# Kernel optimization log

Hardware: AMD Instinct MI355X
Metric: run time of the kernel (lower is better)

## Reference

```python
import jax, jax.numpy as jnp
import numpy as np

N, C, P, K = 100000, 64, 64, 16  # points, in_planes, planes, nsample
EPS = 1e-5

def _bn(y, g, b, m, v):
    # inference-mode batchnorm over channel (last) dim
    return (y - m) * (g * jax.lax.rsqrt(v + EPS)) + b

def setup_inputs() -> dict:
    key = jax.random.key(0)
    ks = jax.random.split(key, 12)
    p = jax.random.normal(ks[0], (N, 3), jnp.float32)
    x = jax.random.normal(ks[1], (N, C), jnp.float32)
    idx = jax.random.randint(ks[2], (N, K), 0, N, jnp.int32)
    s = 0.05
    w1 = jax.random.normal(ks[3], (C, P), jnp.float32) * s
    conv_w = jax.random.normal(ks[4], (P, P + 3), jnp.float32) * s  # Conv1d(P+3, P, 1) weight squeezed
    w3 = jax.random.normal(ks[5], (P, P), jnp.float32) * s
    def bn_params(k):
        k1, k2 = jax.random.split(k)
        return (jnp.ones((P,), jnp.float32),                      # gamma
                jnp.zeros((P,), jnp.float32),                     # beta
                jax.random.normal(k1, (P,), jnp.float32) * 0.01,  # running mean
                jnp.abs(jax.random.normal(k2, (P,), jnp.float32)) * 0.1 + 1.0)  # running var
    g1, b1, m1, v1 = bn_params(ks[6])
    g2, b2, m2, v2 = bn_params(ks[7])
    g3, b3, m3, v3 = bn_params(ks[8])
    return dict(p=p, x=x, idx=idx, w1=w1, g1=g1, b1=b1, m1=m1, v1=v1,
                conv_w=conv_w, g2=g2, b2=b2, m2=m2, v2=v2,
                w3=w3, g3=g3, b3=b3, m3=m3, v3=v3)

def reference(p, x, idx, w1, g1, b1, m1, v1, conv_w, g2, b2, m2, v2, w3, g3, b3, m3, v3):
    identity = x
    h = jax.nn.relu(_bn(x @ w1, g1, b1, m1, v1))                     # [N, P]
    # queryandgroup with use_xyz=True: concat(relative xyz, neighbor feats)
    rel = p[idx] - p[:, None, :]                                      # [N, K, 3]
    grouped = jnp.concatenate([rel, h[idx]], axis=-1)                 # [N, K, 3+P]
    e = jnp.einsum('nkc,oc->nko', grouped, conv_w)                    # conv1x1 -> [N, K, P]
    e = jax.nn.relu(_bn(e, g2, b2, m2, v2))
    f = jnp.max(e, axis=1)                                            # max over neighbors -> [N, P]
    out = jax.nn.relu(_bn(f @ w3, g3, b3, m3, v3) + identity)         # [N, P]
    return out
```

## Files before the change

kernel.cpp:

```cpp
#include <hip/hip_runtime.h>
#include <stdint.h>


#define EPS 1e-5f

typedef unsigned short u16;
typedef unsigned int u32;
typedef __attribute__((ext_vector_type(8))) short bf16x8;
typedef __attribute__((ext_vector_type(4))) float f32x4;

__device__ __forceinline__ float b2f(u16 u) { return __uint_as_float(((u32)u) << 16); }
__device__ __forceinline__ u16 f2b(float f) {
    u32 u = __float_as_uint(f);
    u32 r = u + 0x7fffu + ((u >> 16) & 1u);
    return (u16)(r >> 16);
}
__device__ __forceinline__ bool is_bf16(const void* g) { return ((const u32*)g)[0] == 0x3F803F80u; }
__device__ __forceinline__ float ldval(const void* p, size_t i, bool isbf) {
    return isbf ? b2f(((const u16*)p)[i]) : ((const float*)p)[i];
}
#define MFMA16(a, b, c) __builtin_amdgcn_mfma_f32_16x16x32_bf16(a, b, c, 0, 0, 0)

__device__ __forceinline__ bf16x8 asbf(uint4 u) {
    union { uint4 u; bf16x8 b; } c;
    c.u = u;
    return c.b;
}

__device__ __forceinline__ bf16x8 ldrow8(const void* base, size_t row, int coff, bool isbf) {
    if (isbf) {
        const u16* pp = (const u16*)base + row * 64 + coff;
        return asbf(*(const uint4*)pp);
    } else {
        const float* pp = (const float*)base + row * 64 + coff;
        float4 q0 = ((const float4*)pp)[0], q1 = ((const float4*)pp)[1];
        bf16x8 r;
        r[0] = (short)f2b(q0.x); r[1] = (short)f2b(q0.y);
        r[2] = (short)f2b(q0.z); r[3] = (short)f2b(q0.w);
        r[4] = (short)f2b(q1.x); r[5] = (short)f2b(q1.y);
        r[6] = (short)f2b(q1.z); r[7] = (short)f2b(q1.w);
        return r;
    }
}

__global__ void __launch_bounds__(256)
k_prep(const void* __restrict__ w1, const void* __restrict__ cw, const void* __restrict__ w3,
       const void* __restrict__ g1, const void* __restrict__ b1, const void* __restrict__ m1,
       const void* __restrict__ v1, const void* __restrict__ g2, const void* __restrict__ b2,
       const void* __restrict__ m2, const void* __restrict__ v2, const void* __restrict__ g3,
       const void* __restrict__ b3, const void* __restrict__ m3, const void* __restrict__ v3,
       uint4* __restrict__ w1f, uint4* __restrict__ cwf, uint4* __restrict__ w3f,
       float* __restrict__ bnst) {
    const bool isbf = is_bf16(g1);
    const int tid = blockIdx.x * blockDim.x + threadIdx.x;
    if (tid < 512) {
        int f = tid >> 6, lane = tid & 63;
        int ch = f >> 2, t = f & 3, quad = lane >> 4, c0 = lane & 15;
        union { uint4 u; bf16x8 b; } r;
#pragma unroll
        for (int j = 0; j < 8; ++j) {
            int c = ch * 32 + quad * 8 + j, o = t * 16 + c0;
            r.b[j] = (short)f2b(ldval(w1, (size_t)c * 64 + o, isbf));
        }
        w1f[f * 64 + lane] = r.u;
    } else if (tid < 1280) {
        int f = (tid - 512) >> 6, lane = tid & 63;
        int ch = f >> 2, t = f & 3, quad = lane >> 4, c0 = lane & 15;
        union { uint4 u; bf16x8 b; } r;
#pragma unroll
        for (int j = 0; j < 8; ++j) {
            int o = t * 16 + c0;
            short val;
            if (ch < 2) {
                int c = ch * 32 + quad * 8 + j;
                val = (short)f2b(ldval(cw, (size_t)o * 67 + 3 + c, isbf));
            } else {
                int pc = quad * 8 + j;
                val = (pc < 3) ? (short)f2b(ldval(cw, (size_t)o * 67 + pc, isbf)) : (short)0;
            }
            r.b[j] = val;
        }
        cwf[f * 64 + lane] = r.u;
    } else if (tid < 1792) {
        int f = (tid - 1280) >> 6, lane = tid & 63;
        int ch = f >> 2, t = f & 3, quad = lane >> 4, c0 = lane & 15;
        union { uint4 u; bf16x8 b; } r;
#pragma unroll
        for (int j = 0; j < 8; ++j) {
            int c = ch * 32 + quad * 8 + j, o = t * 16 + c0;
            r.b[j] = (short)f2b(ldval(w3, (size_t)c * 64 + o, isbf));
        }
        w3f[f * 64 + lane] = r.u;
    } else if (tid < 2176) {
        int id = tid - 1792;
        int bn = id >> 7, rem = id & 127, ch = rem & 63, which = rem >> 6;
        const void* g = (bn == 0) ? g1 : (bn == 1) ? g2 : g3;
        const void* b = (bn == 0) ? b1 : (bn == 1) ? b2 : b3;
        const void* m = (bn == 0) ? m1 : (bn == 1) ? m2 : m3;
        const void* v = (bn == 0) ? v1 : (bn == 1) ? v2 : v3;
        float gv = ldval(g, ch, isbf), bv = ldval(b, ch, isbf);
        float mv = ldval(m, ch, isbf), vv = ldval(v, ch, isbf);
        float s = gv * rsqrtf(vv + EPS);
        float t = bv - mv * s;
        bnst[bn * 128 + which * 64 + ch] = which ? t : s;
    }
}

__global__ void __launch_bounds__(256, 4)
k_h_mfma(const void* __restrict__ x, const void* __restrict__ p, const void* __restrict__ g1,
         const uint4* __restrict__ w1f, const float* __restrict__ bnst,
         float4* __restrict__ p4, u16* __restrict__ hbf, int N) {
    const bool isbf = is_bf16(g1);
    const int lane = threadIdx.x & 63, quad = lane >> 4, col = lane & 15;
    const int wave = blockIdx.x * (blockDim.x >> 6) + (threadIdx.x >> 6);
    const int nw = gridDim.x * (blockDim.x >> 6);
    bf16x8 B00 = asbf(w1f[0 * 64 + lane]), B01 = asbf(w1f[1 * 64 + lane]);
    bf16x8 B02 = asbf(w1f[2 * 64 + lane]), B03 = asbf(w1f[3 * 64 + lane]);
    bf16x8 B10 = asbf(w1f[4 * 64 + lane]), B11 = asbf(w1f[5 * 64 + lane]);
    bf16x8 B12 = asbf(w1f[6 * 64 + lane]), B13 = asbf(w1f[7 * 64 + lane]);
    f32x4 sv, tv;
#pragma unroll
    for (int t = 0; t < 4; ++t) {
        sv[t] = bnst[0 * 128 + 0 + t * 16 + col];
        tv[t] = bnst[0 * 128 + 64 + t * 16 + col];
    }
    const int nt = (N + 15) >> 4;
    for (int ti = wave; ti < nt; ti += nw) {
        const int n0 = ti * 16;
        int ra = n0 + col;
        if (ra > N - 1) ra = N - 1;
        bf16x8 A0 = ldrow8(x, (size_t)ra, quad * 8, isbf);
        bf16x8 A1 = ldrow8(x, (size_t)ra, 32 + quad * 8, isbf);
        if (quad == 0 && n0 + col < N) {
            int row = n0 + col;
            float4 pv;
            pv.x = ldval(p, (size_t)row * 3 + 0, isbf);
            pv.y = ldval(p, (size_t)row * 3 + 1, isbf);
            pv.z = ldval(p, (size_t)row * 3 + 2, isbf);
            pv.w = 0.f;
            p4[row] = pv;
        }
        f32x4 acc0 = {0.f, 0.f, 0.f, 0.f}, acc1 = acc0, acc2 = acc0, acc3 = acc0;
        acc0 = MFMA16(A0, B00, acc0); acc0 = MFMA16(A1, B10, acc0);
        acc1 = MFMA16(A0, B01, acc1); acc1 = MFMA16(A1, B11, acc1);
        acc2 = MFMA16(A0, B02, acc2); acc2 = MFMA16(A1, B12, acc2);
        acc3 = MFMA16(A0, B03, acc3); acc3 = MFMA16(A1, B13, acc3);
#define STT(acc, t)                                                            \
    {                                                                          \
        _Pragma("unroll") for (int r = 0; r < 4; ++r) {                        \
            int row = n0 + quad * 4 + r;                                       \
            if (row < N) {                                                     \
                float e = acc[r] * sv[t] + tv[t];                              \
                hbf[(size_t)row * 64 + (t)*16 + col] = f2b(fmaxf(e, 0.f));     \
            }                                                                  \
        }                                                                      \
    }
        STT(acc0, 0) STT(acc1, 1) STT(acc2, 2) STT(acc3, 3)
#undef STT
    }
}

template <bool FORCE_BF16>
__global__ void __launch_bounds__(256, 3)
k_conv_mfma(const u16* __restrict__ hbf, const float4* __restrict__ p4,
            const int* __restrict__ idx, const uint4* __restrict__ cwf,
            const float* __restrict__ bnst, const void* __restrict__ g2,
            void* __restrict__ fout, int N) {
    const bool isbf = is_bf16(g2);
    const int lane = threadIdx.x & 63, quad = lane >> 4, col = lane & 15;
    const int wave = blockIdx.x * (blockDim.x >> 6) + (threadIdx.x >> 6);
    const int nw = gridDim.x * (blockDim.x >> 6);
    bf16x8 B00 = asbf(cwf[0 * 64 + lane]), B01 = asbf(cwf[1 * 64 + lane]);
    bf16x8 B02 = asbf(cwf[2 * 64 + lane]), B03 = asbf(cwf[3 * 64 + lane]);
    bf16x8 B10 = asbf(cwf[4 * 64 + lane]), B11 = asbf(cwf[5 * 64 + lane]);
    bf16x8 B12 = asbf(cwf[6 * 64 + lane]), B13 = asbf(cwf[7 * 64 + lane]);
    bf16x8 B20 = asbf(cwf[8 * 64 + lane]), B21 = asbf(cwf[9 * 64 + lane]);
    bf16x8 B22 = asbf(cwf[10 * 64 + lane]), B23 = asbf(cwf[11 * 64 + lane]);
    f32x4 sv, tv;
#pragma unroll
    for (int t = 0; t < 4; ++t) {
        sv[t] = bnst[1 * 128 + 0 + t * 16 + col];
        tv[t] = bnst[1 * 128 + 64 + t * 16 + col];
    }
    const int step = 2 * nw;
    int b = 2 * wave;
    int ja_c = 0, jb_c = 0;
    uint4 h0a_c, h1a_c, h0b_c, h1b_c;
    if (b < N) {
        const int na = b, nb = (b + 1 < N) ? b + 1 : b;
        ja_c = idx[(size_t)na * 16 + col];
        jb_c = idx[(size_t)nb * 16 + col];
        const uint4* ra = (const uint4*)(hbf + (size_t)ja_c * 64);
        const uint4* rb = (const uint4*)(hbf + (size_t)jb_c * 64);
        h0a_c = ra[quad]; h1a_c = ra[4 + quad];
        h0b_c = rb[quad]; h1b_c = rb[4 + quad];
    }
    for (; b < N; b += step) {
        const int bnext = b + step;
        int ja_n = 0, jb_n = 0;
        uint4 h0a_n = {0, 0, 0, 0}, h1a_n = h0a_n, h0b_n = h0a_n, h1b_n = h0a_n;
        if (bnext < N) {
            const int na = bnext, nb = (bnext + 1 < N) ? bnext + 1 : bnext;
            ja_n = idx[(size_t)na * 16 + col];
            jb_n = idx[(size_t)nb * 16 + col];
            const uint4* ra = (const uint4*)(hbf + (size_t)ja_n * 64);
            const uint4* rb = (const uint4*)(hbf + (size_t)jb_n * 64);
            h0a_n = ra[quad]; h1a_n = ra[4 + quad];
            h0b_n = rb[quad]; h1b_n = rb[4 + quad];
        }
        const int na = b, nb = (b + 1 < N) ? b + 1 : b;
        float4 pja = p4[ja_c], pjb = p4[jb_c];
        float4 pna = p4[na], pnb = p4[nb];
        bf16x8 A2a = {0, 0, 0, 0, 0, 0, 0, 0}, A2b = A2a;
        if (quad == 0) {
            A2a[0] = (short)f2b(pja.x - pna.x);
            A2a[1] = (short)f2b(pja.y - pna.y);
            A2a[2] = (short)f2b(pja.z - pna.z);
            A2b[0] = (short)f2b(pjb.x - pnb.x);
            A2b[1] = (short)f2b(pjb.y - pnb.y);
            A2b[2] = (short)f2b(pjb.z - pnb.z);
        }
        f32x4 z = {0.f, 0.f, 0.f, 0.f};
        f32x4 acc0a = z, acc1a = z, acc2a = z, acc3a = z;
        f32x4 acc0b = z, acc1b = z, acc2b = z, acc3b = z;
        bf16x8 a0a = asbf(h0a_c), a1a = asbf(h1a_c);
        bf16x8 a0b = asbf(h0b_c), a1b = asbf(h1b_c);
        acc0a = MFMA16(a0a, B00, acc0a); acc0b = MFMA16(a0b, B00, acc0b);
        acc1a = MFMA16(a0a, B01, acc1a); acc1b = MFMA16(a0b, B01, acc1b);
        acc2a = MFMA16(a0a, B02, acc2a); acc2b = MFMA16(a0b, B02, acc2b);
        acc3a = MFMA16(a0a, B03, acc3a); acc3b = MFMA16(a0b, B03, acc3b);
        acc0a = MFMA16(a1a, B10, acc0a); acc0b = MFMA16(a1b, B10, acc0b);
        acc1a = MFMA16(a1a, B11, acc1a); acc1b = MFMA16(a1b, B11, acc1b);
        acc2a = MFMA16(a1a, B12, acc2a); acc2b = MFMA16(a1b, B12, acc2b);
        acc3a = MFMA16(a1a, B13, acc3a); acc3b = MFMA16(a1b, B13, acc3b);
        acc0a = MFMA16(A2a, B20, acc0a); acc0b = MFMA16(A2b, B20, acc0b);
        acc1a = MFMA16(A2a, B21, acc1a); acc1b = MFMA16(A2b, B21, acc1b);
        acc2a = MFMA16(A2a, B22, acc2a); acc2b = MFMA16(A2b, B22, acc2b);
        acc3a = MFMA16(A2a, B23, acc3a); acc3b = MFMA16(A2b, B23, acc3b);
#define RED(acc, t, dst)                                                       \
    {                                                                          \
        float mx = fmaxf(fmaxf(acc[0], acc[1]), fmaxf(acc[2], acc[3]));        \
        float mn = fminf(fminf(acc[0], acc[1]), fminf(acc[2], acc[3]));        \
        mx = fmaxf(mx, __shfl_xor(mx, 16));                                    \
        mn = fminf(mn, __shfl_xor(mn, 16));                                    \
        mx = fmaxf(mx, __shfl_xor(mx, 32));                                    \
        mn = fminf(mn, __shfl_xor(mn, 32));                                    \
        float e = fmaxf(sv[t] * mx + tv[t], sv[t] * mn + tv[t]);               \
        dst = fmaxf(e, 0.f);                                                   \
    }
        {
            float f0, f1, f2, f3;
            RED(acc0a, 0, f0) RED(acc1a, 1, f1) RED(acc2a, 2, f2) RED(acc3a, 3, f3)
            float fv = (lane < 16) ? f0 : (lane < 32) ? f1 : (lane < 48) ? f2 : f3;
            if (FORCE_BF16 || isbf)
                ((u16*)fout)[(size_t)na * 64 + lane] = f2b(fv);
            else
                ((float*)fout)[(size_t)na * 64 + lane] = fv;
        }
        if (b + 1 < N) {
            float f0, f1, f2, f3;
            RED(acc0b, 0, f0) RED(acc1b, 1, f1) RED(acc2b, 2, f2) RED(acc3b, 3, f3)
            float fv = (lane < 16) ? f0 : (lane < 32) ? f1 : (lane < 48) ? f2 : f3;
            if (FORCE_BF16 || isbf)
                ((u16*)fout)[(size_t)nb * 64 + lane] = f2b(fv);
            else
                ((float*)fout)[(size_t)nb * 64 + lane] = fv;
        }
#undef RED
        ja_c = ja_n; jb_c = jb_n;
        h0a_c = h0a_n; h1a_c = h1a_n; h0b_c = h0b_n; h1b_c = h1b_n;
    }
}

template <bool FIN_BF16_ALWAYS>
__global__ void __launch_bounds__(256, 4)
k_out_mfma(const void* __restrict__ fin, const void* __restrict__ x,
           const uint4* __restrict__ w3f, const float* __restrict__ bnst,
           const void* __restrict__ g3, void* __restrict__ out, int N) {
    const bool isbf = is_bf16(g3);
    const bool finbf = FIN_BF16_ALWAYS ? true : isbf;
    const int lane = threadIdx.x & 63, quad = lane >> 4, col = lane & 15;
    const int wave = blockIdx.x * (blockDim.x >> 6) + (threadIdx.x >> 6);
    const int nw = gridDim.x * (blockDim.x >> 6);
    bf16x8 B00 = asbf(w3f[0 * 64 + lane]), B01 = asbf(w3f[1 * 64 + lane]);
    bf16x8 B02 = asbf(w3f[2 * 64 + lane]), B03 = asbf(w3f[3 * 64 + lane]);
    bf16x8 B10 = asbf(w3f[4 * 64 + lane]), B11 = asbf(w3f[5 * 64 + lane]);
    bf16x8 B12 = asbf(w3f[6 * 64 + lane]), B13 = asbf(w3f[7 * 64 + lane]);
    f32x4 sv, tv;
#pragma unroll
    for (int t = 0; t < 4; ++t) {
        sv[t] = bnst[2 * 128 + 0 + t * 16 + col];
        tv[t] = bnst[2 * 128 + 64 + t * 16 + col];
    }
    const int nt = (N + 15) >> 4;
    for (int ti = wave; ti < nt; ti += nw) {
        const int n0 = ti * 16;
        int ra = n0 + col;
        if (ra > N - 1) ra = N - 1;
        bf16x8 A0 = ldrow8(fin, (size_t)ra, quad * 8, finbf);
        bf16x8 A1 = ldrow8(fin, (size_t)ra, 32 + quad * 8, finbf);
        f32x4 acc0 = {0.f, 0.f, 0.f, 0.f}, acc1 = acc0, acc2 = acc0, acc3 = acc0;
        acc0 = MFMA16(A0, B00, acc0); acc0 = MFMA16(A1, B10, acc0);
        acc1 = MFMA16(A0, B01, acc1); acc1 = MFMA16(A1, B11, acc1);
        acc2 = MFMA16(A0, B02, acc2); acc2 = MFMA16(A1, B12, acc2);
        acc3 = MFMA16(A0, B03, acc3); acc3 = MFMA16(A1, B13, acc3);
#define STT(acc, t)                                                            \
    {                                                                          \
        _Pragma("unroll") for (int r = 0; r < 4; ++r) {                        \
            int row = n0 + quad * 4 + r;                                       \
            if (row < N) {                                                     \
                int o_ = (t)*16 + col;                                         \
                float e = acc[r] * sv[t] + tv[t] +                             \
                          ldval(x, (size_t)row * 64 + o_, isbf);               \
                e = fmaxf(e, 0.f);                                             \
                if (isbf)                                                      \
                    ((u16*)out)[(size_t)row * 64 + o_] = f2b(e);               \
                else                                                           \
                    ((float*)out)[(size_t)row * 64 + o_] = e;                  \
            }                                                                  \
        }                                                                      \
    }
        STT(acc0, 0) STT(acc1, 1) STT(acc2, 2) STT(acc3, 3)
#undef STT
    }
}

__device__ __forceinline__ void load_col64(const void* w, int lane, bool isbf, float* col) {
#pragma unroll
    for (int c = 0; c < 64; ++c) col[c] = ldval(w, (size_t)c * 64 + lane, isbf);
}
__device__ __forceinline__ float dot64(const void* x, size_t off, bool isbf, const float* col) {
    float a0 = 0.f;
#pragma unroll
    for (int c = 0; c < 64; ++c) a0 += ldval(x, off + c, isbf) * col[c];
    return a0;
}
__device__ __forceinline__ void bn_st(const void* g, const void* b, const void* m,
                                      const void* v, int o, bool isbf, float& s, float& t) {
    float gv = ldval(g, o, isbf), bv = ldval(b, o, isbf);
    float mv = ldval(m, o, isbf), vv = ldval(v, o, isbf);
    s = gv * rsqrtf(vv + EPS);
    t = bv - mv * s;
}
__global__ void __launch_bounds__(256) k_mono(const void* __restrict__ p, const void* __restrict__ x,
                                              const int* __restrict__ idx, const void* __restrict__ w1,
                                              const void* __restrict__ g1, const void* __restrict__ b1,
                                              const void* __restrict__ m1, const void* __restrict__ v1,
                                              const void* __restrict__ cw, const void* __restrict__ g2,
                                              const void* __restrict__ b2, const void* __restrict__ m2,
                                              const void* __restrict__ v2, const void* __restrict__ w3,
                                              const void* __restrict__ g3, const void* __restrict__ b3,
                                              const void* __restrict__ m3, const void* __restrict__ v3,
                                              void* __restrict__ out, int N) {
    const bool isbf = is_bf16(g1);
    const int lane = threadIdx.x & 63;
    const int wave = blockIdx.x * (blockDim.x >> 6) + (threadIdx.x >> 6);
    const int nw = gridDim.x * (blockDim.x >> 6);
    float w1col[64];
    load_col64(w1, lane, isbf, w1col);
    float w3col[64];
    load_col64(w3, lane, isbf, w3col);
    float s1, t1, s2, t2, s3, t3;
    bn_st(g1, b1, m1, v1, lane, isbf, s1, t1);
    bn_st(g2, b2, m2, v2, lane, isbf, s2, t2);
    bn_st(g3, b3, m3, v3, lane, isbf, s3, t3);
    for (int n = wave; n < N; n += nw) {
        const int4* ir = (const int4*)(idx + (size_t)n * 16);
        float pnx = ldval(p, (size_t)n * 3 + 0, isbf);
        float pny = ldval(p, (size_t)n * 3 + 1, isbf);
        float pnz = ldval(p, (size_t)n * 3 + 2, isbf);
        float fmx = 0.f;
        for (int kk = 0; kk < 4; ++kk) {
            const int4 iv = ir[kk];
#pragma unroll
            for (int t = 0; t < 4; ++t) {
                const int j = (t == 0) ? iv.x : (t == 1) ? iv.y : (t == 2) ? iv.z : iv.w;
                float hr = dot64(x, (size_t)j * 64, isbf, w1col);
                float hv = fmaxf(hr * s1 + t1, 0.f);
                float a0 = (ldval(p, (size_t)j * 3 + 0, isbf) - pnx) * ldval(cw, (size_t)lane * 67 + 0, isbf) +
                           (ldval(p, (size_t)j * 3 + 1, isbf) - pny) * ldval(cw, (size_t)lane * 67 + 1, isbf) +
                           (ldval(p, (size_t)j * 3 + 2, isbf) - pnz) * ldval(cw, (size_t)lane * 67 + 2, isbf);
#pragma unroll
                for (int c = 0; c < 64; ++c)
                    a0 += __shfl(hv, c) * ldval(cw, (size_t)lane * 67 + 3 + c, isbf);
                fmx = fmaxf(fmx, a0 * s2 + t2);
            }
        }
        float a = 0.f;
#pragma unroll
        for (int c = 0; c < 64; ++c) a += __shfl(fmx, c) * w3col[c];
        float r = a * s3 + t3 + ldval(x, (size_t)n * 64 + lane, isbf);
        r = fmaxf(r, 0.f);
        if (isbf)
            ((u16*)out)[(size_t)n * 64 + lane] = f2b(r);
        else
            ((float*)out)[(size_t)n * 64 + lane] = r;
    }
}

extern "C" void kernel_launch(void* const* d_in, const int* in_sizes, int n_in,
                              void* d_out, int out_size, void* d_ws, size_t ws_size,
                              hipStream_t stream) {
    const void* p = d_in[0];
    const void* x = d_in[1];
    const int* idx = (const int*)d_in[2];
    const void* w1 = d_in[3];
    const void* g1 = d_in[4];
    const void* b1 = d_in[5];
    const void* m1 = d_in[6];
    const void* v1 = d_in[7];
    const void* cw = d_in[8];
    const void* g2 = d_in[9];
    const void* b2 = d_in[10];
    const void* m2 = d_in[11];
    const void* v2 = d_in[12];
    const void* w3 = d_in[13];
    const void* g3 = d_in[14];
    const void* b3 = d_in[15];
    const void* m3 = d_in[16];
    const void* v3 = d_in[17];
    const int N = in_sizes[0] / 3;

    const int blk = 256;
    const int nt = (N + 15) >> 4;
    const int gh = (nt + 3) >> 2;
    const int gc = 1536;

    const size_t hb = (size_t)N * 64 * sizeof(u16);
    const size_t p4b = (size_t)N * sizeof(float4);
    const size_t packb = 8192 + 12288 + 8192 + 1536;
    const size_t need_hf = 256 + 2 * hb + p4b + packb;
    const size_t need_h = 256 + hb + p4b + packb;

    if (ws_size >= need_h) {
        char* base = (char*)d_ws + 256;
        const bool big = (ws_size >= need_hf);
        u16* h = (u16*)base;
        u16* f = big ? (u16*)(base + hb) : nullptr;
        char* rest = base + (big ? 2 * hb : hb);
        float4* p4 = (float4*)rest;
        uint4* w1f = (uint4*)(rest + p4b);
        uint4* cwf = (uint4*)(rest + p4b + 8192);
        uint4* w3f = (uint4*)(rest + p4b + 8192 + 12288);
        float* bnst = (float*)(rest + p4b + 8192 + 12288 + 8192);
        k_prep<<<9, blk, 0, stream>>>(w1, cw, w3, g1, b1, m1, v1, g2, b2, m2, v2,
                                      g3, b3, m3, v3, w1f, cwf, w3f, bnst);
        k_h_mfma<<<gh, blk, 0, stream>>>(x, p, g1, w1f, bnst, p4, h, N);
        if (big) {
            k_conv_mfma<true><<<gc, blk, 0, stream>>>(h, p4, idx, cwf, bnst, g2, (void*)f, N);
            k_out_mfma<true><<<gh, blk, 0, stream>>>((const void*)f, x, w3f, bnst, g3, d_out, N);
        } else {
            k_conv_mfma<false><<<gc, blk, 0, stream>>>(h, p4, idx, cwf, bnst, g2, d_out, N);
            k_out_mfma<false><<<gh, blk, 0, stream>>>((const void*)d_out, x, w3f, bnst, g3, d_out, N);
        }
    } else {
        k_mono<<<2048, blk, 0, stream>>>(p, x, idx, w1, g1, b1, m1, v1, cw, g2, b2, m2, v2,
                                         w3, g3, b3, m3, v3, d_out, N);
    }
}
```

Measured before the change: 185.4 us.

## Restructure conv gather loop into one-point three-stage prefetch pipeline

The grouped-conv kernel now handles one point per wave per iteration instead of two. It uses a deeper software pipeline: neighbor indices are loaded two iterations ahead, and feature rows plus xyz are loaded one iteration ahead. Fewer live registers allow raising launch bounds to 4 blocks per SM and the grid to 2048 blocks, trading per-wave ILP for more waves in flight to hide gather latency. The risk is less MFMA interleaving per wave and a longer idx→row dependency chain.

```diff
diff --git a/kernel.cpp b/kernel.cpp
--- a/kernel.cpp
+++ b/kernel.cpp
@@ -161,7 +161,7 @@
 }
 
 template <bool FORCE_BF16>
-__global__ void __launch_bounds__(256, 3)
+__global__ void __launch_bounds__(256, 4)
 k_conv_mfma(const u16* __restrict__ hbf, const float4* __restrict__ p4,
             const int* __restrict__ idx, const uint4* __restrict__ cwf,
             const float* __restrict__ bnst, const void* __restrict__ g2,
@@ -182,61 +182,47 @@
         sv[t] = bnst[1 * 128 + 0 + t * 16 + col];
         tv[t] = bnst[1 * 128 + 64 + t * 16 + col];
     }
-    const int step = 2 * nw;
-    int b = 2 * wave;
-    int ja_c = 0, jb_c = 0;
-    uint4 h0a_c, h1a_c, h0b_c, h1b_c;
-    if (b < N) {
-        const int na = b, nb = (b + 1 < N) ? b + 1 : b;
-        ja_c = idx[(size_t)na * 16 + col];
-        jb_c = idx[(size_t)nb * 16 + col];
-        const uint4* ra = (const uint4*)(hbf + (size_t)ja_c * 64);
-        const uint4* rb = (const uint4*)(hbf + (size_t)jb_c * 64);
-        h0a_c = ra[quad]; h1a_c = ra[4 + quad];
-        h0b_c = rb[quad]; h1b_c = rb[4 + quad];
-    }
-    for (; b < N; b += step) {
-        const int bnext = b + step;
-        int ja_n = 0, jb_n = 0;
-        uint4 h0a_n = {0, 0, 0, 0}, h1a_n = h0a_n, h0b_n = h0a_n, h1b_n = h0a_n;
-        if (bnext < N) {
-            const int na = bnext, nb = (bnext + 1 < N) ? bnext + 1 : bnext;
-            ja_n = idx[(size_t)na * 16 + col];
-            jb_n = idx[(size_t)nb * 16 + col];
-            const uint4* ra = (const uint4*)(hbf + (size_t)ja_n * 64);
-            const uint4* rb = (const uint4*)(hbf + (size_t)jb_n * 64);
-            h0a_n = ra[quad]; h1a_n = ra[4 + quad];
-            h0b_n = rb[quad]; h1b_n = rb[4 + quad];
-        }
-        const int na = b, nb = (b + 1 < N) ? b + 1 : b;
-        float4 pja = p4[ja_c], pjb = p4[jb_c];
-        float4 pna = p4[na], pnb = p4[nb];
-        bf16x8 A2a = {0, 0, 0, 0, 0, 0, 0, 0}, A2b = A2a;
+    int i = wave;
+    if (i >= N) return;
+    const int step = nw;
+    int i1 = i + step;
+    int i1c = (i1 < N) ? i1 : N - 1;
+    int j0 = idx[(size_t)i * 16 + col];
+    int j1 = idx[(size_t)i1c * 16 + col];
+    const uint4* r0 = (const uint4*)(hbf + (size_t)j0 * 64);
+    uint4 h0_c = r0[quad], h1_c = r0[4 + quad];
+    float4 pj_c = p4[j0];
+    float4 pn_c = p4[i];
+    for (; i < N; i += step, i1 += step) {
+        const int i2 = i1 + step;
+        const int i2c = (i2 < N) ? i2 : N - 1;
+        int j2 = idx[(size_t)i2c * 16 + col];
+        const uint4* rn = (const uint4*)(hbf + (size_t)j1 * 64);
+        uint4 h0_n = rn[quad], h1_n = rn[4 + quad];
+        const int i1cc = (i1 < N) ? i1 : N - 1;
+        float4 pj_n = p4[j1];
+        float4 pn_n = p4[i1cc];
+        bf16x8 A2 = {0, 0, 0, 0, 0, 0, 0, 0};
         if (quad == 0) {
-            A2a[0] = (short)f2b(pja.x - pna.x);
-            A2a[1] = (short)f2b(pja.y - pna.y);
-            A2a[2] = (short)f2b(pja.z - pna.z);
-            A2b[0] = (short)f2b(pjb.x - pnb.x);
-            A2b[1] = (short)f2b(pjb.y - pnb.y);
-            A2b[2] = (short)f2b(pjb.z - pnb.z);
+            A2[0] = (short)f2b(pj_c.x - pn_c.x);
+            A2[1] = (short)f2b(pj_c.y - pn_c.y);
+            A2[2] = (short)f2b(pj_c.z - pn_c.z);
         }
         f32x4 z = {0.f, 0.f, 0.f, 0.f};
-        f32x4 acc0a = z, acc1a = z, acc2a = z, acc3a = z;
-        f32x4 acc0b = z, acc1b = z, acc2b = z, acc3b = z;
-        bf16x8 a0a = asbf(h0a_c), a1a = asbf(h1a_c);
-        bf16x8 a0b = asbf(h0b_c), a1b = asbf(h1b_c);
-        acc0a = MFMA16(a0a, B00, acc0a); acc0b = MFMA16(a0b, B00, acc0b);
-        acc1a = MFMA16(a0a, B01, acc1a); acc1b = MFMA16(a0b, B01, acc1b);
-        acc2a = MFMA16(a0a, B02, acc2a); acc2b = MFMA16(a0b, B02, acc2b);
-        acc3a = MFMA16(a0a, B03, acc3a); acc3b = MFMA16(a0b, B03, acc3b);
-        acc0a = MFMA16(a1a, B10, acc0a); acc0b = MFMA16(a1b, B10, acc0b);
-        acc1a = MFMA16(a1a, B11, acc1a); acc1b = MFMA16(a1b, B11, acc1b);
-        acc2a = MFMA16(a1a, B12, acc2a); acc2b = MFMA16(a1b, B12, acc2b);
-        acc3a = MFMA16(a1a, B13, acc3a); acc3b = MFMA16(a1b, B13, acc3b);
-        acc0a = MFMA16(A2a, B20, acc0a); acc0b = MFMA16(A2b, B20, acc0b);
-        acc1a = MFMA16(A2a, B21, acc1a); acc1b = MFMA16(A2b, B21, acc1b);
-        acc2a = MFMA16(A2a, B22, acc2a); acc2b = MFMA16(A2b, B22, acc2b);
-        acc3a = MFMA16(A2a, B23, acc3a); acc3b = MFMA16(A2b, B23, acc3b);
+        f32x4 acc0 = z, acc1 = z, acc2 = z, acc3 = z;
+        bf16x8 a0 = asbf(h0_c), a1 = asbf(h1_c);
+        acc0 = MFMA16(a0, B00, acc0);
+        acc1 = MFMA16(a0, B01, acc1);
+        acc2 = MFMA16(a0, B02, acc2);
+        acc3 = MFMA16(a0, B03, acc3);
+        acc0 = MFMA16(a1, B10, acc0);
+        acc1 = MFMA16(a1, B11, acc1);
+        acc2 = MFMA16(a1, B12, acc2);
+        acc3 = MFMA16(a1, B13, acc3);
+        acc0 = MFMA16(A2, B20, acc0);
+        acc1 = MFMA16(A2, B21, acc1);
+        acc2 = MFMA16(A2, B22, acc2);
+        acc3 = MFMA16(A2, B23, acc3);
 #define RED(acc, t, dst)                                                       \
     {                                                                          \
         float mx = fmaxf(fmaxf(acc[0], acc[1]), fmaxf(acc[2], acc[3]));        \
@@ -248,27 +234,17 @@
         float e = fmaxf(sv[t] * mx + tv[t], sv[t] * mn + tv[t]);               \
         dst = fmaxf(e, 0.f);                                                   \
     }
-        {
-            float f0, f1, f2, f3;
-            RED(acc0a, 0, f0) RED(acc1a, 1, f1) RED(acc2a, 2, f2) RED(acc3a, 3, f3)
-            float fv = (lane < 16) ? f0 : (lane < 32) ? f1 : (lane < 48) ? f2 : f3;
-            if (FORCE_BF16 || isbf)
-                ((u16*)fout)[(size_t)na * 64 + lane] = f2b(fv);
-            else
-                ((float*)fout)[(size_t)na * 64 + lane] = fv;
-        }
-        if (b + 1 < N) {
-            float f0, f1, f2, f3;
-            RED(acc0b, 0, f0) RED(acc1b, 1, f1) RED(acc2b, 2, f2) RED(acc3b, 3, f3)
-            float fv = (lane < 16) ? f0 : (lane < 32) ? f1 : (lane < 48) ? f2 : f3;
-            if (FORCE_BF16 || isbf)
-                ((u16*)fout)[(size_t)nb * 64 + lane] = f2b(fv);
-            else
-                ((float*)fout)[(size_t)nb * 64 + lane] = fv;
-        }
+        float f0, f1, f2, f3;
+        RED(acc0, 0, f0) RED(acc1, 1, f1) RED(acc2, 2, f2) RED(acc3, 3, f3)
 #undef RED
-        ja_c = ja_n; jb_c = jb_n;
-        h0a_c = h0a_n; h1a_c = h1a_n; h0b_c = h0b_n; h1b_c = h1b_n;
+        float fv = (lane < 16) ? f0 : (lane < 32) ? f1 : (lane < 48) ? f2 : f3;
+        if (FORCE_BF16 || isbf)
+            ((u16*)fout)[(size_t)i * 64 + lane] = f2b(fv);
+        else
+            ((float*)fout)[(size_t)i * 64 + lane] = fv;
+        j0 = j1; j1 = j2;
+        h0_c = h0_n; h1_c = h1_n;
+        pj_c = pj_n; pn_c = pn_n;
     }
 }
 
@@ -424,7 +400,7 @@
     const int blk = 256;
     const int nt = (N + 15) >> 4;
     const int gh = (nt + 3) >> 2;
-    const int gc = 1536;
+    const int gc = 2048;
 
     const size_t hb = (size_t)N * 64 * sizeof(u16);
     const size_t p4b = (size_t)N * sizeof(float4);
```

Measured after the change: 177.4 us. 4.3% less time.
